# Kernel tuning notes

Hardware: AMD Instinct MI355X
Metric: run time of the kernel (lower is better)

The kernel has to match this reference:

```python
import jax, jax.numpy as jnp
import numpy as np

B, C, N, K, COUT = 8, 128, 10000, 16, 256


def setup_inputs() -> dict:
    key = jax.random.key(0)
    ks = jax.random.split(key, 8)
    x = jax.random.normal(ks[0], (B, C, N, 1), dtype=jnp.float32)
    edge_index = jax.random.randint(ks[1], (2, B, N, K), 0, N)
    s1 = 1.0 / np.sqrt(C)
    W1 = jax.random.uniform(ks[2], (C, C), jnp.float32, -s1, s1)   # nn1 1x1 conv weight
    b1 = jax.random.uniform(ks[3], (C,), jnp.float32, -s1, s1)
    Wp = jax.random.uniform(ks[4], (C, C), jnp.float32, -s1, s1)   # nn_pooling Linear
    bp = jax.random.uniform(ks[5], (C,), jnp.float32, -s1, s1)
    s2 = 1.0 / np.sqrt(2 * C)
    W2 = jax.random.uniform(ks[6], (COUT, 2 * C), jnp.float32, -s2, s2)  # nn2 1x1 conv
    b2 = jax.random.uniform(ks[7], (COUT,), jnp.float32, -s2, s2)
    return dict(x=x, edge_index=edge_index, W1=W1, b1=b1, Wp=Wp, bp=bp, W2=W2, b2=b2)


def reference(x, edge_index, W1, b1, Wp, bp, W2, b2):
    b, c, n, _ = x.shape
    k = edge_index.shape[-1]
    # nn1: 1x1 conv (channel mix) + ReLU -> [B,C,N,1]
    h = jax.nn.relu(jnp.einsum('bcns,dc->bdns', x, W1) + b1[None, :, None, None])
    # batched_index_select: gather neighbor features along vertex dim -> [B,C,N,K]
    hn = h[:, :, :, 0]                              # [B,C,N]
    idx = edge_index[0].reshape(b, 1, n * k)        # broadcast over C
    xj = jnp.take_along_axis(hn, idx, axis=2).reshape(b, c, n, k)
    # nn_pooling: Linear over channel dim + ReLU (transpose(1,3) in torch == act on C)
    xj = jax.nn.relu(jnp.einsum('bcnk,dc->bdnk', xj, Wp) + bp[None, :, None, None])
    # max-pool over neighbors, keepdim -> [B,C,N,1]
    xj = jnp.max(xj, axis=-1, keepdims=True)
    # concat along channels, nn2: 1x1 conv + ReLU -> [B,COUT,N,1]
    cat = jnp.concatenate([h, xj], axis=1)
    out = jax.nn.relu(jnp.einsum('bcns,dc->bdns', cat, W2) + b2[None, :, None, None])
    return out
```

## Files before the change

kernel.cpp:

```cpp
#include <hip/hip_runtime.h>

#define NODES 10000
#define BATCH 8
#define CH    128
#define KNB   16
#define CO    256

typedef __bf16 bf16x8 __attribute__((ext_vector_type(8)));
typedef float  f32x4  __attribute__((ext_vector_type(4)));

__device__ __forceinline__ unsigned short f2bf(float f) {
  unsigned u = __float_as_uint(f);
  u = (u + 0x7FFFu + ((u >> 16) & 1u)) >> 16;
  return (unsigned short)u;
}

__device__ __forceinline__ unsigned pkmax(unsigned a, unsigned b) {
  unsigned d;
  asm("v_pk_max_u16 %0, %1, %2" : "=v"(d) : "v"(a), "v"(b));
  return d;
}
__device__ __forceinline__ uint4 pkmax4(uint4 a, uint4 b) {
  a.x = pkmax(a.x, b.x); a.y = pkmax(a.y, b.y);
  a.z = pkmax(a.z, b.z); a.w = pkmax(a.w, b.w);
  return a;
}
__device__ __forceinline__ bf16x8 asbf8(uint4 u) {
  union { uint4 u; bf16x8 b; } c; c.u = u; return c.b;
}

__device__ __forceinline__ void gload_lds16(const void* g, void* l) {
  __builtin_amdgcn_global_load_lds(
      (const __attribute__((address_space(1))) unsigned int*)g,
      (__attribute__((address_space(3))) unsigned int*)l, 16, 0, 0);
}

__global__ __launch_bounds__(256) void prep(
    const float* __restrict__ W1, const float* __restrict__ Wp,
    const float* __restrict__ W2,
    unsigned short* __restrict__ W1b, unsigned short* __restrict__ Wpb,
    unsigned short* __restrict__ W2b)
{
  int i = blockIdx.x * 256 + threadIdx.x;
  const float* src; unsigned short* dst; int off;
  if (i < 4096)      { src = W1; dst = W1b; off = i; }
  else if (i < 8192) { src = Wp; dst = Wpb; off = i - 4096; }
  else               { src = W2; dst = W2b; off = i - 8192; }
  float4 v = ((const float4*)src)[off];
  ushort4 o;
  o.x = f2bf(v.x); o.y = f2bf(v.y); o.z = f2bf(v.z); o.w = f2bf(v.w);
  ((ushort4*)dst)[off] = o;
}

__global__ __launch_bounds__(256) void fused_hz(
    const unsigned short* __restrict__ W1b, const float* __restrict__ b1,
    const unsigned short* __restrict__ Wpb, const float* __restrict__ bp,
    const float* __restrict__ x,
    unsigned short* __restrict__ h_t, unsigned short* __restrict__ z_t)
{
  const int b  = blockIdx.y;
  const int n0 = blockIdx.x * 64;
  const int t  = threadIdx.x;
  const int lane = t & 63, w = t >> 6;
  const int lm = lane & 15, q = lane >> 4;
  const size_t nb = (size_t)b * NODES;

  __shared__ __align__(16) unsigned short Bt[64 * 128];
  __shared__ __align__(16) unsigned short Ht[64 * 128];
  char* BtB = (char*)Bt;
  char* HtB = (char*)Ht;

  {
    const float* X = x + (size_t)b * CH * NODES;
#pragma unroll
    for (int rep = 0; rep < 4; ++rep) {
      int flat = t + rep * 256;
      int c2 = flat >> 4, n4 = flat & 15;
      int c  = c2 * 2;
      int gn = n0 + n4 * 4;
      float4 a0 = make_float4(0.f,0.f,0.f,0.f), a1 = a0;
      if (gn < NODES) {
        a0 = *(const float4*)(X + (size_t)c * NODES + gn);
        a1 = *(const float4*)(X + (size_t)(c + 1) * NODES + gn);
      }
      float v0[4] = {a0.x, a0.y, a0.z, a0.w};
      float v1[4] = {a1.x, a1.y, a1.z, a1.w};
#pragma unroll
      for (int i = 0; i < 4; ++i) {
        int nn = n4 * 4 + i;
        unsigned pk = (unsigned)f2bf(v0[i]) | ((unsigned)f2bf(v1[i]) << 16);
        int phys = nn * 256 + (((c2 >> 2) ^ (nn & 7)) << 4) + ((c2 & 3) << 2);
        *(unsigned*)(BtB + phys) = pk;
      }
    }
  }

  const int d0  = (w & 1) * 64;
  const int nbw = (w >> 1) * 32;

  uint4 af[4][4];
#pragma unroll
  for (int dt = 0; dt < 4; ++dt)
#pragma unroll
    for (int kt = 0; kt < 4; ++kt)
      af[dt][kt] = *(const uint4*)(W1b + (d0 + dt*16 + lm) * CH + kt*32 + q*8);

  __syncthreads();

  f32x4 acc[4][2];
#pragma unroll
  for (int dt = 0; dt < 4; ++dt)
#pragma unroll
    for (int nt = 0; nt < 2; ++nt) acc[dt][nt] = (f32x4){0.f,0.f,0.f,0.f};

#pragma unroll
  for (int kt = 0; kt < 4; ++kt)
#pragma unroll
    for (int nt = 0; nt < 2; ++nt) {
      int nl = nbw + nt * 16 + lm;
      int chunk = kt * 4 + q;
      int phys = nl * 256 + ((chunk ^ (nl & 7)) << 4);
      bf16x8 bb = asbf8(*(const uint4*)(BtB + phys));
#pragma unroll
      for (int dt = 0; dt < 4; ++dt)
        acc[dt][nt] = __builtin_amdgcn_mfma_f32_16x16x32_bf16(
            asbf8(af[dt][kt]), bb, acc[dt][nt], 0, 0, 0);
    }

  uint4 af2[4][4];
#pragma unroll
  for (int dt = 0; dt < 4; ++dt)
#pragma unroll
    for (int kt = 0; kt < 4; ++kt)
      af2[dt][kt] = *(const uint4*)(Wpb + (d0 + dt*16 + lm) * CH + kt*32 + q*8);

#pragma unroll
  for (int dt = 0; dt < 4; ++dt) {
    int dbase = d0 + dt * 16 + q * 4;
    float4 bi = *(const float4*)(b1 + dbase);
    float bv[4] = {bi.x, bi.y, bi.z, bi.w};
#pragma unroll
    for (int nt = 0; nt < 2; ++nt) {
      int nl = nbw + nt * 16 + lm;
      ushort4 o;
      o.x = f2bf(fmaxf(acc[dt][nt][0] + bv[0], 0.f));
      o.y = f2bf(fmaxf(acc[dt][nt][1] + bv[1], 0.f));
      o.z = f2bf(fmaxf(acc[dt][nt][2] + bv[2], 0.f));
      o.w = f2bf(fmaxf(acc[dt][nt][3] + bv[3], 0.f));
      int chunk = dbase >> 3;
      int phys  = nl * 256 + ((chunk ^ (nl & 7)) << 4) + ((q & 1) << 3);
      *(ushort4*)(HtB + phys) = o;
    }
  }

  __syncthreads();

  {
    int nl = t >> 2;
    int gn = n0 + nl;
#pragma unroll
    for (int rep = 0; rep < 4; ++rep) {
      int g = (t & 3) + rep * 4;
      int phys = nl * 256 + ((g ^ (nl & 7)) << 4);
      uint4 v = *(const uint4*)(HtB + phys);
      if (gn < NODES)
        *(uint4*)((char*)h_t + (nb + (size_t)gn) * 256 + g * 16) = v;
    }
  }

#pragma unroll
  for (int dt = 0; dt < 4; ++dt)
#pragma unroll
    for (int nt = 0; nt < 2; ++nt) acc[dt][nt] = (f32x4){0.f,0.f,0.f,0.f};

#pragma unroll
  for (int kt = 0; kt < 4; ++kt)
#pragma unroll
    for (int nt = 0; nt < 2; ++nt) {
      int nl = nbw + nt * 16 + lm;
      int chunk = kt * 4 + q;
      int phys = nl * 256 + ((chunk ^ (nl & 7)) << 4);
      bf16x8 bb = asbf8(*(const uint4*)(HtB + phys));
#pragma unroll
      for (int dt = 0; dt < 4; ++dt)
        acc[dt][nt] = __builtin_amdgcn_mfma_f32_16x16x32_bf16(
            asbf8(af2[dt][kt]), bb, acc[dt][nt], 0, 0, 0);
    }

#pragma unroll
  for (int dt = 0; dt < 4; ++dt) {
    int dbase = d0 + dt * 16 + q * 4;
    float4 bi = *(const float4*)(bp + dbase);
    float bv[4] = {bi.x, bi.y, bi.z, bi.w};
#pragma unroll
    for (int nt = 0; nt < 2; ++nt) {
      int nl = nbw + nt * 16 + lm;
      ushort4 o;
      o.x = f2bf(fmaxf(acc[dt][nt][0] + bv[0], 0.f));
      o.y = f2bf(fmaxf(acc[dt][nt][1] + bv[1], 0.f));
      o.z = f2bf(fmaxf(acc[dt][nt][2] + bv[2], 0.f));
      o.w = f2bf(fmaxf(acc[dt][nt][3] + bv[3], 0.f));
      int chunk = dbase >> 3;
      int phys  = nl * 256 + ((chunk ^ (nl & 7)) << 4) + ((q & 1) << 3);
      *(ushort4*)(BtB + phys) = o;
    }
  }

  __syncthreads();

  {
    int nl = t >> 2;
    int gn = n0 + nl;
#pragma unroll
    for (int rep = 0; rep < 4; ++rep) {
      int g = (t & 3) + rep * 4;
      int phys = nl * 256 + ((g ^ (nl & 7)) << 4);
      uint4 v = *(const uint4*)(BtB + phys);
      if (gn < NODES)
        *(uint4*)((char*)z_t + (nb + (size_t)gn) * 256 + g * 16) = v;
    }
  }
}

__global__ __launch_bounds__(256) void gmax_kernel(
    const unsigned short* __restrict__ z_t, const int* __restrict__ e0,
    unsigned short* __restrict__ zm)
{
  const int bid = blockIdx.x;
  const int b   = bid & 7;
  const int n0  = (bid >> 3) * 64;
  const int t   = threadIdx.x;
  const int nl  = t >> 2, c = t & 3;
  const int gn  = n0 + nl;
  if (gn >= NODES) return;

  const int* ip = e0 + ((size_t)b * NODES + gn) * KNB;
  int4 iv0 = *(const int4*)(ip);
  int4 iv1 = *(const int4*)(ip + 4);
  int4 iv2 = *(const int4*)(ip + 8);
  int4 iv3 = *(const int4*)(ip + 12);
  int idx[16] = {iv0.x, iv0.y, iv0.z, iv0.w,
                 iv1.x, iv1.y, iv1.z, iv1.w,
                 iv2.x, iv2.y, iv2.z, iv2.w,
                 iv3.x, iv3.y, iv3.z, iv3.w};

  const char* Z = (const char*)(z_t + (size_t)b * NODES * CH) + c * 16;
  uint4 m[4];
#pragma unroll
  for (int cg = 0; cg < 4; ++cg) m[cg] = make_uint4(0u, 0u, 0u, 0u);

#pragma unroll
  for (int k = 0; k < KNB; ++k) {
    const char* p = Z + (size_t)idx[k] * (CH * 2);
#pragma unroll
    for (int cg = 0; cg < 4; ++cg)
      m[cg] = pkmax4(m[cg], *(const uint4*)(p + cg * 64));
  }

  char* O = (char*)(zm + ((size_t)b * NODES + gn) * CH) + c * 16;
#pragma unroll
  for (int cg = 0; cg < 4; ++cg)
    *(uint4*)(O + cg * 64) = m[cg];
}

__device__ __forceinline__ void og_stage(
    unsigned short* buf, const unsigned short* __restrict__ h_t,
    const unsigned short* __restrict__ zm, size_t nb, int n0, int w, int lane)
{
#pragma unroll
  for (int rep = 0; rep < 8; ++rep) {
    const int row0 = w * 2 + rep * 8;
    const int nl = row0 + (lane >> 5);
    const int l  = (lane & 31) ^ (nl & 7);
    int gn = n0 + nl; if (gn > NODES - 1) gn = NODES - 1;
    const unsigned short* src = (l < 16)
        ? h_t + (nb + (size_t)gn) * CH + l * 8
        : zm  + (nb + (size_t)gn) * CH + (l - 16) * 8;
    gload_lds16(src, (char*)buf + row0 * 512);
  }
  __builtin_amdgcn_sched_barrier(0);
}

__device__ __forceinline__ void og_mfma(
    f32x4 (&acc)[4][4], const unsigned short* buf,
    const uint4 (&af)[8][4], int lm, int q)
{
  const char* catB = (const char*)buf;
#pragma unroll
  for (int dt = 0; dt < 4; ++dt)
#pragma unroll
    for (int nt = 0; nt < 4; ++nt) acc[dt][nt] = (f32x4){0.f, 0.f, 0.f, 0.f};
#pragma unroll
  for (int kt = 0; kt < 8; ++kt)
#pragma unroll
    for (int nt = 0; nt < 4; ++nt) {
      int nl = nt * 16 + lm;
      int chunk = kt * 4 + q;
      int phys = nl * 512 + ((chunk ^ (nl & 7)) << 4);
      bf16x8 bb = asbf8(*(const uint4*)(catB + phys));
#pragma unroll
      for (int dt = 0; dt < 4; ++dt)
        acc[dt][nt] = __builtin_amdgcn_mfma_f32_16x16x32_bf16(
            asbf8(af[kt][dt]), bb, acc[dt][nt], 0, 0, 0);
    }
}

__device__ __forceinline__ void og_epi(
    const f32x4 (&acc)[4][4], const float* __restrict__ b2,
    float* __restrict__ out, int b, int n0, int w, int lm, int q)
{
  const int d0 = w * 64;
#pragma unroll
  for (int dt = 0; dt < 4; ++dt) {
    int dbase = d0 + dt * 16 + q * 4;
    float4 bi = *(const float4*)(b2 + dbase);
    float bv[4] = {bi.x, bi.y, bi.z, bi.w};
#pragma unroll
    for (int nt = 0; nt < 4; ++nt) {
      int gn = n0 + nt * 16 + lm;
      if (gn < NODES) {
        float* op = out + ((size_t)(b * CO + dbase) * NODES) + gn;
#pragma unroll
        for (int r = 0; r < 4; ++r)
          op[(size_t)r * NODES] = fmaxf(acc[dt][nt][r] + bv[r], 0.f);
      }
    }
  }
}

__global__ __launch_bounds__(256) void out_gemm(
    const unsigned short* __restrict__ h_t, const unsigned short* __restrict__ zm,
    const unsigned short* __restrict__ W2b, const float* __restrict__ b2,
    float* __restrict__ out)
{
  const int bid = blockIdx.x;
  const int b   = bid & 7;
  const int g   = bid >> 3;
  const int t   = threadIdx.x;
  const int lane = t & 63, w = t >> 6;
  const int lm = lane & 15, q = lane >> 4;
  const size_t nb = (size_t)b * NODES;

  __shared__ __align__(16) unsigned short bufA[64 * 256];
  __shared__ __align__(16) unsigned short bufB[64 * 256];

  const int d0 = w * 64;
  uint4 af[8][4];
#pragma unroll
  for (int kt = 0; kt < 8; ++kt)
#pragma unroll
    for (int dt = 0; dt < 4; ++dt)
      af[kt][dt] = *(const uint4*)(W2b + (d0 + dt*16 + lm) * CO + kt*32 + q*8);

  const int n0_0 = g * 64;
  const int n0_1 = (g + 64) * 64;
  const int n0_2 = (g + 128) * 64;
  const bool has2 = (g + 128) < 157;

  f32x4 acc[4][4];

  og_stage(bufA, h_t, zm, nb, n0_0, w, lane);
  asm volatile("s_waitcnt vmcnt(0)" ::: "memory");
  __builtin_amdgcn_sched_barrier(0);
  __builtin_amdgcn_s_barrier();

  og_stage(bufB, h_t, zm, nb, n0_1, w, lane);
  og_mfma(acc, bufA, af, lm, q);
  asm volatile("s_waitcnt vmcnt(0)" ::: "memory");
  __builtin_amdgcn_sched_barrier(0);
  __builtin_amdgcn_s_barrier();
  og_epi(acc, b2, out, b, n0_0, w, lm, q);

  if (has2) {
    og_stage(bufA, h_t, zm, nb, n0_2, w, lane);
    og_mfma(acc, bufB, af, lm, q);
    asm volatile("s_waitcnt vmcnt(0)" ::: "memory");
    __builtin_amdgcn_sched_barrier(0);
    __builtin_amdgcn_s_barrier();
    og_epi(acc, b2, out, b, n0_1, w, lm, q);
    og_mfma(acc, bufA, af, lm, q);
    og_epi(acc, b2, out, b, n0_2, w, lm, q);
  } else {
    og_mfma(acc, bufB, af, lm, q);
    og_epi(acc, b2, out, b, n0_1, w, lm, q);
  }
}

extern "C" void kernel_launch(void* const* d_in, const int* in_sizes, int n_in,
                              void* d_out, int out_size, void* d_ws, size_t ws_size,
                              hipStream_t stream) {
  const float* x  = (const float*)d_in[0];
  const int*   ei = (const int*)d_in[1];
  const float* W1 = (const float*)d_in[2];
  const float* b1 = (const float*)d_in[3];
  const float* Wp = (const float*)d_in[4];
  const float* bp = (const float*)d_in[5];
  const float* W2 = (const float*)d_in[6];
  const float* b2 = (const float*)d_in[7];
  float* out = (float*)d_out;

  unsigned short* ws  = (unsigned short*)d_ws;
  unsigned short* h_t = ws;
  unsigned short* z_t = h_t + (size_t)BATCH * NODES * CH;
  unsigned short* W1b = z_t + (size_t)BATCH * NODES * CH;
  unsigned short* Wpb = W1b + CH * CH;
  unsigned short* W2b = Wpb + CH * CH;
  unsigned short* zm  = W2b + CO * 2 * CH;

  prep<<<96, 256, 0, stream>>>(W1, Wp, W2, W1b, Wpb, W2b);

  const int NT = (NODES + 63) / 64;
  fused_hz<<<dim3(NT, BATCH), 256, 0, stream>>>(W1b, b1, Wpb, bp, x, h_t, z_t);
  gmax_kernel<<<BATCH * NT, 256, 0, stream>>>(z_t, ei, zm);
  out_gemm<<<512, 256, 0, stream>>>(h_t, zm, W2b, b2, out);
}
```

Before: 199.0 us.

## Split x transpose into its own kernel and double-buffer persistent fused_hz

Moves the fp32-to-bf16 transpose of x into a separate prep_x kernel that writes a node-major bf16 copy to workspace. fused_hz becomes a persistent grid of 512 blocks. Each block loads both weight fragment sets once and walks up to three node tiles, using direct global-to-LDS loads into two alternating buffers so the next tile's load overlaps the current tile's MFMA work. This is meant to hide load latency and amortise the weight register loads, at the cost of an extra kernel launch, an extra round trip of x through global memory, and higher LDS use per block.

```diff
diff --git a/kernel.cpp b/kernel.cpp
--- a/kernel.cpp
+++ b/kernel.cpp
@@ -52,60 +52,84 @@
   ((ushort4*)dst)[off] = o;
 }
 
-__global__ __launch_bounds__(256) void fused_hz(
-    const unsigned short* __restrict__ W1b, const float* __restrict__ b1,
-    const unsigned short* __restrict__ Wpb, const float* __restrict__ bp,
-    const float* __restrict__ x,
-    unsigned short* __restrict__ h_t, unsigned short* __restrict__ z_t)
+__global__ __launch_bounds__(256) void prep_x(
+    const float* __restrict__ x, unsigned short* __restrict__ x_t)
 {
   const int b  = blockIdx.y;
   const int n0 = blockIdx.x * 64;
   const int t  = threadIdx.x;
-  const int lane = t & 63, w = t >> 6;
-  const int lm = lane & 15, q = lane >> 4;
   const size_t nb = (size_t)b * NODES;
 
   __shared__ __align__(16) unsigned short Bt[64 * 128];
-  __shared__ __align__(16) unsigned short Ht[64 * 128];
   char* BtB = (char*)Bt;
+
+  const float* X = x + (size_t)b * CH * NODES;
+#pragma unroll
+  for (int rep = 0; rep < 4; ++rep) {
+    int flat = t + rep * 256;
+    int c2 = flat >> 4, n4 = flat & 15;
+    int c  = c2 * 2;
+    int gn = n0 + n4 * 4;
+    float4 a0 = make_float4(0.f,0.f,0.f,0.f), a1 = a0;
+    if (gn < NODES) {
+      a0 = *(const float4*)(X + (size_t)c * NODES + gn);
+      a1 = *(const float4*)(X + (size_t)(c + 1) * NODES + gn);
+    }
+    float v0[4] = {a0.x, a0.y, a0.z, a0.w};
+    float v1[4] = {a1.x, a1.y, a1.z, a1.w};
+#pragma unroll
+    for (int i = 0; i < 4; ++i) {
+      int nn = n4 * 4 + i;
+      unsigned pk = (unsigned)f2bf(v0[i]) | ((unsigned)f2bf(v1[i]) << 16);
+      int phys = nn * 256 + (((c2 >> 2) ^ (nn & 7)) << 4) + ((c2 & 3) << 2);
+      *(unsigned*)(BtB + phys) = pk;
+    }
+  }
+  __syncthreads();
+
+  {
+    int nl = t >> 2;
+    int gn = n0 + nl;
+#pragma unroll
+    for (int rep = 0; rep < 4; ++rep) {
+      int g = (t & 3) + rep * 4;
+      int phys = nl * 256 + ((g ^ (nl & 7)) << 4);
+      uint4 v = *(const uint4*)(BtB + phys);
+      if (gn < NODES)
+        *(uint4*)((char*)x_t + (nb + (size_t)gn) * 256 + g * 16) = v;
+    }
+  }
+}
+
+__device__ __forceinline__ void hz_stage(
+    unsigned short* buf, const unsigned short* __restrict__ x_t,
+    size_t nb, int n0, int w, int lane)
+{
+#pragma unroll
+  for (int rep = 0; rep < 4; ++rep) {
+    const int row0 = w * 16 + rep * 4;
+    const int nl = row0 + (lane >> 4);
+    const int c  = lane & 15;
+    const int l  = c ^ (nl & 7);
+    int gn = n0 + nl; if (gn > NODES - 1) gn = NODES - 1;
+    const unsigned short* src = x_t + (nb + (size_t)gn) * CH + l * 8;
+    gload_lds16(src, (char*)buf + row0 * 256);
+  }
+  __builtin_amdgcn_sched_barrier(0);
+}
+
+__device__ __forceinline__ void hz_compute(
+    const unsigned short* buf, unsigned short* Ht, unsigned short* Zt,
+    const uint4 (&af)[4][4], const uint4 (&af2)[4][4],
+    const float* __restrict__ b1, const float* __restrict__ bp,
+    unsigned short* __restrict__ h_t, unsigned short* __restrict__ z_t,
+    size_t nb, int n0, int t, int w, int lm, int q)
+{
+  const char* BtB = (const char*)buf;
   char* HtB = (char*)Ht;
-
-  {
-    const float* X = x + (size_t)b * CH * NODES;
-#pragma unroll
-    for (int rep = 0; rep < 4; ++rep) {
-      int flat = t + rep * 256;
-      int c2 = flat >> 4, n4 = flat & 15;
-      int c  = c2 * 2;
-      int gn = n0 + n4 * 4;
-      float4 a0 = make_float4(0.f,0.f,0.f,0.f), a1 = a0;
-      if (gn < NODES) {
-        a0 = *(const float4*)(X + (size_t)c * NODES + gn);
-        a1 = *(const float4*)(X + (size_t)(c + 1) * NODES + gn);
-      }
-      float v0[4] = {a0.x, a0.y, a0.z, a0.w};
-      float v1[4] = {a1.x, a1.y, a1.z, a1.w};
-#pragma unroll
-      for (int i = 0; i < 4; ++i) {
-        int nn = n4 * 4 + i;
-        unsigned pk = (unsigned)f2bf(v0[i]) | ((unsigned)f2bf(v1[i]) << 16);
-        int phys = nn * 256 + (((c2 >> 2) ^ (nn & 7)) << 4) + ((c2 & 3) << 2);
-        *(unsigned*)(BtB + phys) = pk;
-      }
-    }
-  }
-
+  char* ZtB = (char*)Zt;
   const int d0  = (w & 1) * 64;
   const int nbw = (w >> 1) * 32;
-
-  uint4 af[4][4];
-#pragma unroll
-  for (int dt = 0; dt < 4; ++dt)
-#pragma unroll
-    for (int kt = 0; kt < 4; ++kt)
-      af[dt][kt] = *(const uint4*)(W1b + (d0 + dt*16 + lm) * CH + kt*32 + q*8);
-
-  __syncthreads();
 
   f32x4 acc[4][2];
 #pragma unroll
@@ -126,13 +150,6 @@
         acc[dt][nt] = __builtin_amdgcn_mfma_f32_16x16x32_bf16(
             asbf8(af[dt][kt]), bb, acc[dt][nt], 0, 0, 0);
     }
-
-  uint4 af2[4][4];
-#pragma unroll
-  for (int dt = 0; dt < 4; ++dt)
-#pragma unroll
-    for (int kt = 0; kt < 4; ++kt)
-      af2[dt][kt] = *(const uint4*)(Wpb + (d0 + dt*16 + lm) * CH + kt*32 + q*8);
 
 #pragma unroll
   for (int dt = 0; dt < 4; ++dt) {
@@ -202,7 +219,7 @@
       o.w = f2bf(fmaxf(acc[dt][nt][3] + bv[3], 0.f));
       int chunk = dbase >> 3;
       int phys  = nl * 256 + ((chunk ^ (nl & 7)) << 4) + ((q & 1) << 3);
-      *(ushort4*)(BtB + phys) = o;
+      *(ushort4*)(ZtB + phys) = o;
     }
   }
 
@@ -215,10 +232,68 @@
     for (int rep = 0; rep < 4; ++rep) {
       int g = (t & 3) + rep * 4;
       int phys = nl * 256 + ((g ^ (nl & 7)) << 4);
-      uint4 v = *(const uint4*)(BtB + phys);
+      uint4 v = *(const uint4*)(ZtB + phys);
       if (gn < NODES)
         *(uint4*)((char*)z_t + (nb + (size_t)gn) * 256 + g * 16) = v;
     }
+  }
+}
+
+__global__ __launch_bounds__(256) void fused_hz(
+    const unsigned short* __restrict__ W1b, const float* __restrict__ b1,
+    const unsigned short* __restrict__ Wpb, const float* __restrict__ bp,
+    const unsigned short* __restrict__ x_t,
+    unsigned short* __restrict__ h_t, unsigned short* __restrict__ z_t)
+{
+  const int bid = blockIdx.x;
+  const int b   = bid & 7;
+  const int g   = bid >> 3;
+  const int t   = threadIdx.x;
+  const int lane = t & 63, w = t >> 6;
+  const int lm = lane & 15, q = lane >> 4;
+  const size_t nb = (size_t)b * NODES;
+
+  __shared__ __align__(16) unsigned short bufA[64 * 128];
+  __shared__ __align__(16) unsigned short bufB[64 * 128];
+  __shared__ __align__(16) unsigned short Ht[64 * 128];
+  __shared__ __align__(16) unsigned short Zt[64 * 128];
+
+  const int d0 = (w & 1) * 64;
+
+  uint4 af[4][4], af2[4][4];
+#pragma unroll
+  for (int dt = 0; dt < 4; ++dt)
+#pragma unroll
+    for (int kt = 0; kt < 4; ++kt) {
+      af[dt][kt]  = *(const uint4*)(W1b + (d0 + dt*16 + lm) * CH + kt*32 + q*8);
+      af2[dt][kt] = *(const uint4*)(Wpb + (d0 + dt*16 + lm) * CH + kt*32 + q*8);
+    }
+
+  const int n0_0 = g * 64;
+  const int n0_1 = (g + 64) * 64;
+  const int n0_2 = (g + 128) * 64;
+  const bool has2 = (g + 128) < 157;
+
+  hz_stage(bufA, x_t, nb, n0_0, w, lane);
+  asm volatile("s_waitcnt vmcnt(0)" ::: "memory");
+  __builtin_amdgcn_sched_barrier(0);
+  __builtin_amdgcn_s_barrier();
+
+  hz_stage(bufB, x_t, nb, n0_1, w, lane);
+  hz_compute(bufA, Ht, Zt, af, af2, b1, bp, h_t, z_t, nb, n0_0, t, w, lm, q);
+  asm volatile("s_waitcnt vmcnt(0)" ::: "memory");
+  __builtin_amdgcn_sched_barrier(0);
+  __builtin_amdgcn_s_barrier();
+
+  if (has2) {
+    hz_stage(bufA, x_t, nb, n0_2, w, lane);
+    hz_compute(bufB, Ht, Zt, af, af2, b1, bp, h_t, z_t, nb, n0_1, t, w, lm, q);
+    asm volatile("s_waitcnt vmcnt(0)" ::: "memory");
+    __builtin_amdgcn_sched_barrier(0);
+    __builtin_amdgcn_s_barrier();
+    hz_compute(bufA, Ht, Zt, af, af2, b1, bp, h_t, z_t, nb, n0_2, t, w, lm, q);
+  } else {
+    hz_compute(bufB, Ht, Zt, af, af2, b1, bp, h_t, z_t, nb, n0_1, t, w, lm, q);
   }
 }
 
@@ -406,11 +481,13 @@
   unsigned short* Wpb = W1b + CH * CH;
   unsigned short* W2b = Wpb + CH * CH;
   unsigned short* zm  = W2b + CO * 2 * CH;
+  unsigned short* x_t = zm  + (size_t)BATCH * NODES * CH;
 
   prep<<<96, 256, 0, stream>>>(W1, Wp, W2, W1b, Wpb, W2b);
 
   const int NT = (NODES + 63) / 64;
-  fused_hz<<<dim3(NT, BATCH), 256, 0, stream>>>(W1b, b1, Wpb, bp, x, h_t, z_t);
+  prep_x<<<dim3(NT, BATCH), 256, 0, stream>>>(x, x_t);
+  fused_hz<<<512, 256, 0, stream>>>(W1b, b1, Wpb, bp, x_t, h_t, z_t);
   gmax_kernel<<<BATCH * NT, 256, 0, stream>>>(z_t, ei, zm);
   out_gemm<<<512, 256, 0, stream>>>(h_t, zm, W2b, b2, out);
 }
```

Result: faster. 194.8 us (-2.1%).

## Make fused_hz per-wave independent and reorder out_gemm epilogue overlap

Applied to the files above, without the earlier changes.

Restructures fused_hz so that each wave owns 16 nodes and all 128 output channels, with private LDS buffers. This removes every __syncthreads from the kernel. Weight fragments are now streamed from global memory one 16-row tile ahead instead of being held in registers. The grid is flattened with batch as the fastest index, and out_gemm moves its first epilogue after the next stage's loads are issued, with a partial vmcnt wait so stores overlap with loads. The trade-off is more repeated weight loads per wave, plus a waitcnt count that depends on how many loads the stage issues.

```diff
diff --git a/kernel.cpp b/kernel.cpp
--- a/kernel.cpp
+++ b/kernel.cpp
@@ -58,166 +58,146 @@
     const float* __restrict__ x,
     unsigned short* __restrict__ h_t, unsigned short* __restrict__ z_t)
 {
-  const int b  = blockIdx.y;
-  const int n0 = blockIdx.x * 64;
-  const int t  = threadIdx.x;
+  const int bid = blockIdx.x;
+  const int b   = bid & 7;
+  const int g   = bid >> 3;
+  const int t   = threadIdx.x;
   const int lane = t & 63, w = t >> 6;
   const int lm = lane & 15, q = lane >> 4;
+  const int n0w = g * 64 + w * 16;
+  if (n0w >= NODES) return;
   const size_t nb = (size_t)b * NODES;
-
-  __shared__ __align__(16) unsigned short Bt[64 * 128];
-  __shared__ __align__(16) unsigned short Ht[64 * 128];
-  char* BtB = (char*)Bt;
-  char* HtB = (char*)Ht;
+  const float* X = x + (size_t)b * CH * NODES;
+
+  __shared__ __align__(16) unsigned short SB[4][2][16 * 128];
+  char* Bt = (char*)SB[w][0];
+  char* Ht = (char*)SB[w][1];
 
   {
-    const float* X = x + (size_t)b * CH * NODES;
-#pragma unroll
-    for (int rep = 0; rep < 4; ++rep) {
-      int flat = t + rep * 256;
-      int c2 = flat >> 4, n4 = flat & 15;
+    const int nq = lane & 3;
+    const int cb = lane >> 2;
+#pragma unroll
+    for (int r = 0; r < 4; ++r) {
+      int c2 = r * 16 + cb;
       int c  = c2 * 2;
-      int gn = n0 + n4 * 4;
-      float4 a0 = make_float4(0.f,0.f,0.f,0.f), a1 = a0;
-      if (gn < NODES) {
-        a0 = *(const float4*)(X + (size_t)c * NODES + gn);
-        a1 = *(const float4*)(X + (size_t)(c + 1) * NODES + gn);
+      int gn = n0w + nq * 4;
+      f32x4 a0 = *(const f32x4*)(X + (size_t)c * NODES + gn);
+      f32x4 a1 = *(const f32x4*)(X + (size_t)(c + 1) * NODES + gn);
+#pragma unroll
+      for (int i = 0; i < 4; ++i) {
+        int nn = nq * 4 + i;
+        unsigned pk = (unsigned)f2bf(a0[i]) | ((unsigned)f2bf(a1[i]) << 16);
+        int phys = nn * 256 + (((c2 >> 2) ^ (nn & 7)) << 4) + ((c2 & 3) << 2);
+        *(unsigned*)(Bt + phys) = pk;
       }
-      float v0[4] = {a0.x, a0.y, a0.z, a0.w};
-      float v1[4] = {a1.x, a1.y, a1.z, a1.w};
-#pragma unroll
-      for (int i = 0; i < 4; ++i) {
-        int nn = n4 * 4 + i;
-        unsigned pk = (unsigned)f2bf(v0[i]) | ((unsigned)f2bf(v1[i]) << 16);
-        int phys = nn * 256 + (((c2 >> 2) ^ (nn & 7)) << 4) + ((c2 & 3) << 2);
-        *(unsigned*)(BtB + phys) = pk;
-      }
-    }
-  }
-
-  const int d0  = (w & 1) * 64;
-  const int nbw = (w >> 1) * 32;
-
-  uint4 af[4][4];
-#pragma unroll
-  for (int dt = 0; dt < 4; ++dt)
+    }
+  }
+
+  bf16x8 bb[4];
+#pragma unroll
+  for (int kt = 0; kt < 4; ++kt) {
+    int phys = lm * 256 + (((kt * 4 + q) ^ (lm & 7)) << 4);
+    bb[kt] = asbf8(*(const uint4*)(Bt + phys));
+  }
+
+  f32x4 acc[8];
+  uint4 acur[4], anxt[4];
+#pragma unroll
+  for (int kt = 0; kt < 4; ++kt)
+    acur[kt] = *(const uint4*)(W1b + lm * CH + kt * 32 + q * 8);
+#pragma unroll
+  for (int dt = 0; dt < 8; ++dt) {
+    if (dt < 7) {
+#pragma unroll
+      for (int kt = 0; kt < 4; ++kt)
+        anxt[kt] = *(const uint4*)(W1b + ((dt + 1) * 16 + lm) * CH
+                                   + kt * 32 + q * 8);
+    }
+    acc[dt] = (f32x4){0.f, 0.f, 0.f, 0.f};
 #pragma unroll
     for (int kt = 0; kt < 4; ++kt)
-      af[dt][kt] = *(const uint4*)(W1b + (d0 + dt*16 + lm) * CH + kt*32 + q*8);
-
-  __syncthreads();
-
-  f32x4 acc[4][2];
-#pragma unroll
-  for (int dt = 0; dt < 4; ++dt)
-#pragma unroll
-    for (int nt = 0; nt < 2; ++nt) acc[dt][nt] = (f32x4){0.f,0.f,0.f,0.f};
+      acc[dt] = __builtin_amdgcn_mfma_f32_16x16x32_bf16(
+          asbf8(acur[kt]), bb[kt], acc[dt], 0, 0, 0);
+#pragma unroll
+    for (int kt = 0; kt < 4; ++kt) acur[kt] = anxt[kt];
+  }
+
+#pragma unroll
+  for (int dt = 0; dt < 8; ++dt) {
+    int dbase = dt * 16 + q * 4;
+    float4 bi = *(const float4*)(b1 + dbase);
+    ushort4 o;
+    o.x = f2bf(fmaxf(acc[dt][0] + bi.x, 0.f));
+    o.y = f2bf(fmaxf(acc[dt][1] + bi.y, 0.f));
+    o.z = f2bf(fmaxf(acc[dt][2] + bi.z, 0.f));
+    o.w = f2bf(fmaxf(acc[dt][3] + bi.w, 0.f));
+    int chunk = dbase >> 3;
+    int phys  = lm * 256 + ((chunk ^ (lm & 7)) << 4) + ((q & 1) << 3);
+    *(ushort4*)(Ht + phys) = o;
+  }
+
+  {
+    int nl = lane >> 2;
+    int gn = n0w + nl;
+#pragma unroll
+    for (int r = 0; r < 4; ++r) {
+      int gch = (lane & 3) + r * 4;
+      int phys = nl * 256 + ((gch ^ (nl & 7)) << 4);
+      uint4 v = *(const uint4*)(Ht + phys);
+      *(uint4*)((char*)h_t + (nb + (size_t)gn) * 256 + gch * 16) = v;
+    }
+  }
+
+  bf16x8 hb[4];
+#pragma unroll
+  for (int kt = 0; kt < 4; ++kt) {
+    int phys = lm * 256 + (((kt * 4 + q) ^ (lm & 7)) << 4);
+    hb[kt] = asbf8(*(const uint4*)(Ht + phys));
+  }
 
 #pragma unroll
   for (int kt = 0; kt < 4; ++kt)
-#pragma unroll
-    for (int nt = 0; nt < 2; ++nt) {
-      int nl = nbw + nt * 16 + lm;
-      int chunk = kt * 4 + q;
-      int phys = nl * 256 + ((chunk ^ (nl & 7)) << 4);
-      bf16x8 bb = asbf8(*(const uint4*)(BtB + phys));
-#pragma unroll
-      for (int dt = 0; dt < 4; ++dt)
-        acc[dt][nt] = __builtin_amdgcn_mfma_f32_16x16x32_bf16(
-            asbf8(af[dt][kt]), bb, acc[dt][nt], 0, 0, 0);
-    }
-
-  uint4 af2[4][4];
-#pragma unroll
-  for (int dt = 0; dt < 4; ++dt)
+    acur[kt] = *(const uint4*)(Wpb + lm * CH + kt * 32 + q * 8);
+#pragma unroll
+  for (int dt = 0; dt < 8; ++dt) {
+    if (dt < 7) {
+#pragma unroll
+      for (int kt = 0; kt < 4; ++kt)
+        anxt[kt] = *(const uint4*)(Wpb + ((dt + 1) * 16 + lm) * CH
+                                   + kt * 32 + q * 8);
+    }
+    acc[dt] = (f32x4){0.f, 0.f, 0.f, 0.f};
 #pragma unroll
     for (int kt = 0; kt < 4; ++kt)
-      af2[dt][kt] = *(const uint4*)(Wpb + (d0 + dt*16 + lm) * CH + kt*32 + q*8);
-
-#pragma unroll
-  for (int dt = 0; dt < 4; ++dt) {
-    int dbase = d0 + dt * 16 + q * 4;
-    float4 bi = *(const float4*)(b1 + dbase);
-    float bv[4] = {bi.x, bi.y, bi.z, bi.w};
-#pragma unroll
-    for (int nt = 0; nt < 2; ++nt) {
-      int nl = nbw + nt * 16 + lm;
-      ushort4 o;
-      o.x = f2bf(fmaxf(acc[dt][nt][0] + bv[0], 0.f));
-      o.y = f2bf(fmaxf(acc[dt][nt][1] + bv[1], 0.f));
-      o.z = f2bf(fmaxf(acc[dt][nt][2] + bv[2], 0.f));
-      o.w = f2bf(fmaxf(acc[dt][nt][3] + bv[3], 0.f));
-      int chunk = dbase >> 3;
-      int phys  = nl * 256 + ((chunk ^ (nl & 7)) << 4) + ((q & 1) << 3);
-      *(ushort4*)(HtB + phys) = o;
-    }
-  }
-
-  __syncthreads();
+      acc[dt] = __builtin_amdgcn_mfma_f32_16x16x32_bf16(
+          asbf8(acur[kt]), hb[kt], acc[dt], 0, 0, 0);
+#pragma unroll
+    for (int kt = 0; kt < 4; ++kt) acur[kt] = anxt[kt];
+  }
+
+#pragma unroll
+  for (int dt = 0; dt < 8; ++dt) {
+    int dbase = dt * 16 + q * 4;
+    float4 bi = *(const float4*)(bp + dbase);
+    ushort4 o;
+    o.x = f2bf(fmaxf(acc[dt][0] + bi.x, 0.f));
+    o.y = f2bf(fmaxf(acc[dt][1] + bi.y, 0.f));
+    o.z = f2bf(fmaxf(acc[dt][2] + bi.z, 0.f));
+    o.w = f2bf(fmaxf(acc[dt][3] + bi.w, 0.f));
+    int chunk = dbase >> 3;
+    int phys  = lm * 256 + ((chunk ^ (lm & 7)) << 4) + ((q & 1) << 3);
+    *(ushort4*)(Bt + phys) = o;
+  }
 
   {
-    int nl = t >> 2;
-    int gn = n0 + nl;
-#pragma unroll
-    for (int rep = 0; rep < 4; ++rep) {
-      int g = (t & 3) + rep * 4;
-      int phys = nl * 256 + ((g ^ (nl & 7)) << 4);
-      uint4 v = *(const uint4*)(HtB + phys);
-      if (gn < NODES)
-        *(uint4*)((char*)h_t + (nb + (size_t)gn) * 256 + g * 16) = v;
-    }
-  }
-
-#pragma unroll
-  for (int dt = 0; dt < 4; ++dt)
-#pragma unroll
-    for (int nt = 0; nt < 2; ++nt) acc[dt][nt] = (f32x4){0.f,0.f,0.f,0.f};
-
-#pragma unroll
-  for (int kt = 0; kt < 4; ++kt)
-#pragma unroll
-    for (int nt = 0; nt < 2; ++nt) {
-      int nl = nbw + nt * 16 + lm;
-      int chunk = kt * 4 + q;
-      int phys = nl * 256 + ((chunk ^ (nl & 7)) << 4);
-      bf16x8 bb = asbf8(*(const uint4*)(HtB + phys));
-#pragma unroll
-      for (int dt = 0; dt < 4; ++dt)
-        acc[dt][nt] = __builtin_amdgcn_mfma_f32_16x16x32_bf16(
-            asbf8(af2[dt][kt]), bb, acc[dt][nt], 0, 0, 0);
-    }
-
-#pragma unroll
-  for (int dt = 0; dt < 4; ++dt) {
-    int dbase = d0 + dt * 16 + q * 4;
-    float4 bi = *(const float4*)(bp + dbase);
-    float bv[4] = {bi.x, bi.y, bi.z, bi.w};
-#pragma unroll
-    for (int nt = 0; nt < 2; ++nt) {
-      int nl = nbw + nt * 16 + lm;
-      ushort4 o;
-      o.x = f2bf(fmaxf(acc[dt][nt][0] + bv[0], 0.f));
-      o.y = f2bf(fmaxf(acc[dt][nt][1] + bv[1], 0.f));
-      o.z = f2bf(fmaxf(acc[dt][nt][2] + bv[2], 0.f));
-      o.w = f2bf(fmaxf(acc[dt][nt][3] + bv[3], 0.f));
-      int chunk = dbase >> 3;
-      int phys  = nl * 256 + ((chunk ^ (nl & 7)) << 4) + ((q & 1) << 3);
-      *(ushort4*)(BtB + phys) = o;
-    }
-  }
-
-  __syncthreads();
-
-  {
-    int nl = t >> 2;
-    int gn = n0 + nl;
-#pragma unroll
-    for (int rep = 0; rep < 4; ++rep) {
-      int g = (t & 3) + rep * 4;
-      int phys = nl * 256 + ((g ^ (nl & 7)) << 4);
-      uint4 v = *(const uint4*)(BtB + phys);
-      if (gn < NODES)
-        *(uint4*)((char*)z_t + (nb + (size_t)gn) * 256 + g * 16) = v;
+    int nl = lane >> 2;
+    int gn = n0w + nl;
+#pragma unroll
+    for (int r = 0; r < 4; ++r) {
+      int gch = (lane & 3) + r * 4;
+      int phys = nl * 256 + ((gch ^ (nl & 7)) << 4);
+      uint4 v = *(const uint4*)(Bt + phys);
+      *(uint4*)((char*)z_t + (nb + (size_t)gn) * 256 + gch * 16) = v;
     }
   }
 }
@@ -360,27 +340,28 @@
   f32x4 acc[4][4];
 
   og_stage(bufA, h_t, zm, nb, n0_0, w, lane);
-  asm volatile("s_waitcnt vmcnt(0)" ::: "memory");
+  asm volatile("s_waitcnt vmcnt(0) lgkmcnt(0)" ::: "memory");
   __builtin_amdgcn_sched_barrier(0);
   __builtin_amdgcn_s_barrier();
 
   og_stage(bufB, h_t, zm, nb, n0_1, w, lane);
   og_mfma(acc, bufA, af, lm, q);
-  asm volatile("s_waitcnt vmcnt(0)" ::: "memory");
+  asm volatile("s_waitcnt vmcnt(0) lgkmcnt(0)" ::: "memory");
   __builtin_amdgcn_sched_barrier(0);
   __builtin_amdgcn_s_barrier();
-  og_epi(acc, b2, out, b, n0_0, w, lm, q);
 
   if (has2) {
     og_stage(bufA, h_t, zm, nb, n0_2, w, lane);
+    og_epi(acc, b2, out, b, n0_0, w, lm, q);
     og_mfma(acc, bufB, af, lm, q);
-    asm volatile("s_waitcnt vmcnt(0)" ::: "memory");
+    asm volatile("s_waitcnt vmcnt(56) lgkmcnt(0)" ::: "memory");
     __builtin_amdgcn_sched_barrier(0);
     __builtin_amdgcn_s_barrier();
     og_epi(acc, b2, out, b, n0_1, w, lm, q);
     og_mfma(acc, bufA, af, lm, q);
     og_epi(acc, b2, out, b, n0_2, w, lm, q);
   } else {
+    og_epi(acc, b2, out, b, n0_0, w, lm, q);
     og_mfma(acc, bufB, af, lm, q);
     og_epi(acc, b2, out, b, n0_1, w, lm, q);
   }
@@ -410,7 +391,7 @@
   prep<<<96, 256, 0, stream>>>(W1, Wp, W2, W1b, Wpb, W2b);
 
   const int NT = (NODES + 63) / 64;
-  fused_hz<<<dim3(NT, BATCH), 256, 0, stream>>>(W1b, b1, Wpb, bp, x, h_t, z_t);
+  fused_hz<<<BATCH * NT, 256, 0, stream>>>(W1b, b1, Wpb, bp, x, h_t, z_t);
   gmax_kernel<<<BATCH * NT, 256, 0, stream>>>(z_t, ei, zm);
   out_gemm<<<512, 256, 0, stream>>>(h_t, zm, W2b, b2, out);
 }
```

Measured after the change: 212.1 us. 6.6% more time.
